# Kernel tuning notes

Measured on AMD Instinct MI355X. Metric: run time of the kernel, lower is better.

## Reference

```python
import jax, jax.numpy as jnp
import numpy as np

B, TQ, TK, D, V = 16, 64, 512, 256, 32000


def setup_inputs() -> dict:
    key = jax.random.key(0)
    k = jax.random.split(key, 8)
    return {
        "domainslots": jax.random.normal(k[0], (B, TQ, D), jnp.float32),
        "out_states": jax.random.normal(k[1], (B, TQ, D), jnp.float32),
        "context": jax.random.normal(k[2], (B, TK, D), jnp.float32),
        "context_plain": jax.random.randint(k[3], (B, TK), 0, V, jnp.int64 if jax.config.jax_enable_x64 else jnp.int32),
        "W_state": jax.random.normal(k[4], (D, V), jnp.float32) * 0.02,
        "b_state": jnp.zeros((V,), jnp.float32),
        "W_gen": jax.random.normal(k[5], (3 * D, 1), jnp.float32) * 0.02,
        "b_gen": jnp.zeros((1,), jnp.float32),
    }


def reference(domainslots, out_states, context, context_plain, W_state, b_state, W_gen, b_gen):
    d = out_states.shape[-1]
    # pointer attention: softmax(Q K^T / sqrt(d)) over context  -> [B, TQ, TK]
    scores = jnp.einsum("bqd,bkd->bqk", out_states, context) / jnp.sqrt(jnp.asarray(d, out_states.dtype))
    pointer_attn = jax.nn.softmax(scores, axis=-1)

    # generation distribution over vocab  -> [B, TQ, V]
    p_state_vocab = jax.nn.softmax(out_states @ W_state + b_state, axis=-1)

    # copy distribution: scatter-add attention mass onto source token ids
    b_idx = jnp.arange(B)[:, None, None]           # [B,1,1]
    q_idx = jnp.arange(TQ)[None, :, None]          # [1,TQ,1]
    v_idx = context_plain[:, None, :]              # [B,1,TK] broadcast over TQ
    p_state_ptr = jnp.zeros((B, TQ, V), p_state_vocab.dtype).at[b_idx, q_idx, v_idx].add(pointer_attn)

    # attention-weighted context vector  -> [B, TQ, D]
    context_vec = jnp.einsum("bqk,bkd->bqd", pointer_attn, context)

    # generation gate  -> [B, TQ, 1]
    p_gen_vec = jnp.concatenate([out_states, context_vec, domainslots], axis=-1)
    p_state_gen = jax.nn.sigmoid(p_gen_vec @ W_gen + b_gen)

    p_state_out = p_state_gen * p_state_vocab + (1.0 - p_state_gen) * p_state_ptr
    return jnp.log(p_state_out)
```

## Files before the change

### kernel.cpp

```cpp
#include <hip/hip_runtime.h>
#include <math.h>

typedef short short8 __attribute__((ext_vector_type(8)));
typedef float f32x4 __attribute__((ext_vector_type(4)));

#define B_ 16
#define TQ_ 64
#define TK_ 512
#define D_ 256
#define V_ 32000
#define M_ (B_ * TQ_)

__device__ __forceinline__ unsigned short f2bf(float x) {
    unsigned int u = __float_as_uint(x);
    unsigned int r = (u + 0x7fffu + ((u >> 16) & 1u)) >> 16;
    return (unsigned short)r;
}

__device__ __forceinline__ void gload_lds16(const void* g, void* l) {
    __builtin_amdgcn_global_load_lds(
        (const __attribute__((address_space(1))) void*)g,
        (__attribute__((address_space(3))) void*)l, 16, 0, 0);
}

__global__ __launch_bounds__(256) void dedup_kernel(
    const int* __restrict__ cp, int* __restrict__ nexta, int* __restrict__ leader)
{
    __shared__ __align__(16) int c[TK_];
    const int b = blockIdx.x, tid = threadIdx.x;
    c[tid] = cp[b * TK_ + tid];
    c[tid + 256] = cp[b * TK_ + 256 + tid];
    __syncthreads();
    for (int k = tid; k < TK_; k += 256) {
        const int v = c[k];
        int fm = 1024, nx = 1024;
#pragma unroll 8
        for (int j0 = 0; j0 < TK_; j0 += 4) {
            const int4 q = *(const int4*)&c[j0];
            if (q.x == v) { fm = min(fm, j0);     if (j0     > k) nx = min(nx, j0);     }
            if (q.y == v) { fm = min(fm, j0 + 1); if (j0 + 1 > k) nx = min(nx, j0 + 1); }
            if (q.z == v) { fm = min(fm, j0 + 2); if (j0 + 2 > k) nx = min(nx, j0 + 2); }
            if (q.w == v) { fm = min(fm, j0 + 3); if (j0 + 3 > k) nx = min(nx, j0 + 3); }
        }
        nexta[b * TK_ + k] = (nx < 1024) ? nx : -1;
        leader[b * TK_ + k] = (fm == k) ? 1 : 0;
    }
}

__global__ __launch_bounds__(256) void conv_a_kernel(
    const float* __restrict__ A, unsigned short* __restrict__ Ab)
{
    const int i = (blockIdx.x * 256 + threadIdx.x) * 4;
    const float4 v = *(const float4*)&A[i];
    ushort4 o;
    o.x = f2bf(v.x); o.y = f2bf(v.y); o.z = f2bf(v.z); o.w = f2bf(v.w);
    *(ushort4*)&Ab[i] = o;
}

__global__ __launch_bounds__(256) void conv_w_kernel(
    const float* __restrict__ W, unsigned short* __restrict__ Wt)
{
    __shared__ float tile[64][65];
    const int tid = threadIdx.x;
    const int k0 = (blockIdx.x & 3) * 64;
    const int n0 = (blockIdx.x >> 2) * 64;
#pragma unroll
    for (int i = 0; i < 16; i++) {
        const int r = i * 4 + (tid >> 6), cc = tid & 63;
        tile[r][cc] = W[(k0 + r) * V_ + n0 + cc];
    }
    __syncthreads();
#pragma unroll
    for (int i = 0; i < 4; i++) {
        const int nl = i * 16 + (tid >> 4);
        const int kq = (tid & 15) * 4;
        ushort4 o;
        o.x = f2bf(tile[kq + 0][nl]);
        o.y = f2bf(tile[kq + 1][nl]);
        o.z = f2bf(tile[kq + 2][nl]);
        o.w = f2bf(tile[kq + 3][nl]);
        *(ushort4*)&Wt[(n0 + nl) * D_ + k0 + kq] = o;
    }
}

__global__ __launch_bounds__(256) void conv_c_kernel(
    const float* __restrict__ ctx, unsigned short* __restrict__ Cb,
    unsigned short* __restrict__ Ct)
{
    __shared__ float tile[64][65];
    const int tid = threadIdx.x;
    const int b = blockIdx.x >> 5;
    const int r5 = blockIdx.x & 31;
    const int k0 = (r5 >> 2) * 64;
    const int d0 = (r5 & 3) * 64;
#pragma unroll
    for (int i = 0; i < 16; i++) {
        const int r = i * 4 + (tid >> 6), cc = tid & 63;
        const float v = ctx[((b * TK_) + k0 + r) * D_ + d0 + cc];
        tile[r][cc] = v;
        Cb[((b * TK_) + k0 + r) * D_ + d0 + cc] = f2bf(v);
    }
    __syncthreads();
#pragma unroll
    for (int i = 0; i < 4; i++) {
        const int dl = i * 16 + (tid >> 4);
        const int kq = (tid & 15) * 4;
        ushort4 o;
        o.x = f2bf(tile[kq + 0][dl]);
        o.y = f2bf(tile[kq + 1][dl]);
        o.z = f2bf(tile[kq + 2][dl]);
        o.w = f2bf(tile[kq + 3][dl]);
        *(ushort4*)&Ct[((b * D_) + d0 + dl) * TK_ + k0 + kq] = o;
    }
}

template <int LDA, int LDB, int KTOT>
__global__ __launch_bounds__(256) void gemm_small(
    const unsigned short* __restrict__ A,
    const unsigned short* __restrict__ Bt,
    float* __restrict__ C, int ldc, int nchunks, int btrows, float scale)
{
    __shared__ short Al[64][72];
    __shared__ short Bl[128][72];
    const int tid = threadIdx.x;
    const int b = blockIdx.x / nchunks;
    const int n0 = (blockIdx.x % nchunks) * 128;
    A += (size_t)b * 64 * LDA;
    Bt += (size_t)b * btrows * LDB;
    C += (size_t)b * 64 * ldc;

    const int wid = tid >> 6;
    const int lane = tid & 63;
    const int wm = wid & 1, wn = wid >> 1;
    const int quad = lane >> 4, l15 = lane & 15;

    f32x4 acc[2][4];
#pragma unroll
    for (int i = 0; i < 2; i++)
#pragma unroll
        for (int j = 0; j < 4; j++) acc[i][j] = f32x4{0.f, 0.f, 0.f, 0.f};

    for (int k0 = 0; k0 < KTOT; k0 += 64) {
        __syncthreads();
#pragma unroll
        for (int i = 0; i < 2; i++) {
            const int c = tid + i * 256;
            const int r = c >> 3, kc = (c & 7) * 8;
            *(uint4*)&Al[r][kc] = *(const uint4*)&A[r * LDA + k0 + kc];
        }
#pragma unroll
        for (int i = 0; i < 4; i++) {
            const int c = tid + i * 256;
            const int r = c >> 3, kc = (c & 7) * 8;
            *(uint4*)&Bl[r][kc] = *(const uint4*)&Bt[(n0 + r) * LDB + k0 + kc];
        }
        __syncthreads();
#pragma unroll
        for (int ks = 0; ks < 64; ks += 32) {
            short8 af[2], bf[4];
#pragma unroll
            for (int mt = 0; mt < 2; mt++)
                af[mt] = *(const short8*)&Al[wm * 32 + mt * 16 + l15][ks + quad * 8];
#pragma unroll
            for (int nt = 0; nt < 4; nt++)
                bf[nt] = *(const short8*)&Bl[wn * 64 + nt * 16 + l15][ks + quad * 8];
#pragma unroll
            for (int mt = 0; mt < 2; mt++)
#pragma unroll
                for (int nt = 0; nt < 4; nt++)
                    acc[mt][nt] = __builtin_amdgcn_mfma_f32_16x16x32_bf16(
                        af[mt], bf[nt], acc[mt][nt], 0, 0, 0);
        }
    }
#pragma unroll
    for (int mt = 0; mt < 2; mt++)
#pragma unroll
        for (int nt = 0; nt < 4; nt++)
#pragma unroll
            for (int r = 0; r < 4; r++) {
                const int rl = wm * 32 + mt * 16 + quad * 4 + r;
                const int col = n0 + wn * 64 + nt * 16 + l15;
                C[rl * ldc + col] = acc[mt][nt][r] * scale;
            }
}

__global__ __launch_bounds__(256) void softmax_kernel(
    float* __restrict__ S, unsigned short* __restrict__ Pb)
{
    const int w = threadIdx.x >> 6, lane = threadIdx.x & 63;
    const int row = blockIdx.x * 4 + w;
    float v[8], m = -1e30f;
#pragma unroll
    for (int j = 0; j < 8; j++) { v[j] = S[row * TK_ + lane + 64 * j]; m = fmaxf(m, v[j]); }
#pragma unroll
    for (int off = 32; off; off >>= 1) m = fmaxf(m, __shfl_xor(m, off));
    float s = 0.f;
#pragma unroll
    for (int j = 0; j < 8; j++) { v[j] = __expf(v[j] - m); s += v[j]; }
#pragma unroll
    for (int off = 32; off; off >>= 1) s += __shfl_xor(s, off);
    const float inv = 1.0f / s;
#pragma unroll
    for (int j = 0; j < 8; j++) {
        const float p = v[j] * inv;
        S[row * TK_ + lane + 64 * j] = p;
        Pb[row * TK_ + lane + 64 * j] = f2bf(p);
    }
}

__global__ __launch_bounds__(256) void pgen_kernel(
    const float* __restrict__ os, const float* __restrict__ cv,
    const float* __restrict__ dm, const float* __restrict__ W_gen,
    const float* __restrict__ b_gen, float* __restrict__ pg)
{
    const int w = threadIdx.x >> 6, lane = threadIdx.x & 63;
    const int row = blockIdx.x * 4 + w;
    const int d4 = lane * 4;
    const float4 o4 = *(const float4*)&os[row * D_ + d4];
    const float4 c4 = *(const float4*)&cv[row * D_ + d4];
    const float4 m4 = *(const float4*)&dm[row * D_ + d4];
    const float4 w0 = *(const float4*)&W_gen[d4];
    const float4 w1 = *(const float4*)&W_gen[D_ + d4];
    const float4 w2 = *(const float4*)&W_gen[2 * D_ + d4];
    float p = o4.x * w0.x + o4.y * w0.y + o4.z * w0.z + o4.w * w0.w
            + c4.x * w1.x + c4.y * w1.y + c4.z * w1.z + c4.w * w1.w
            + m4.x * w2.x + m4.y * w2.y + m4.z * w2.z + m4.w * w2.w;
#pragma unroll
    for (int off = 32; off; off >>= 1) p += __shfl_xor(p, off);
    if (lane == 0) pg[row] = 1.0f / (1.0f + __expf(-(p + b_gen[0])));
}

__global__ __launch_bounds__(256) void gemm_vocab_z(
    const unsigned short* __restrict__ A,
    const unsigned short* __restrict__ Bt,
    const float* __restrict__ b_state,
    float* __restrict__ Z)
{
    __shared__ short Al[128][64];
    __shared__ short Bl[128][64];
    __shared__ float bst[128];

    const int tid = threadIdx.x;
    const int swz = (blockIdx.x & 7) * 250 + (blockIdx.x >> 3);
    const int m0 = (swz & 7) * 128;
    const int n0 = (swz >> 3) * 128;

    if (tid < 128) bst[tid] = b_state[n0 + tid];

    const int wid = tid >> 6, lane = tid & 63;
    const int wm = wid & 1, wn = wid >> 1;
    const int quad = lane >> 4, l15 = lane & 15;
    const int srow = lane >> 3;
    const int scolz = ((lane & 7) ^ srow) << 3;

    f32x4 acc[4][4];
#pragma unroll
    for (int i = 0; i < 4; i++)
#pragma unroll
        for (int j = 0; j < 4; j++) acc[i][j] = f32x4{0.f, 0.f, 0.f, 0.f};

    for (int k0 = 0; k0 < D_; k0 += 64) {
        __syncthreads();
#pragma unroll
        for (int j = 0; j < 4; j++) {
            const int c = j * 4 + wid;
            const int r = c * 8 + srow;
            gload_lds16(&A[(size_t)(m0 + r) * D_ + k0 + scolz], &Al[c * 8][0]);
        }
#pragma unroll
        for (int j = 0; j < 4; j++) {
            const int c = j * 4 + wid;
            const int r = c * 8 + srow;
            gload_lds16(&Bt[(size_t)(n0 + r) * D_ + k0 + scolz], &Bl[c * 8][0]);
        }
        __syncthreads();
#pragma unroll
        for (int ks = 0; ks < 64; ks += 32) {
            short8 af[4], bf[4];
#pragma unroll
            for (int mt = 0; mt < 4; mt++) {
                const int row = wm * 64 + mt * 16 + l15;
                af[mt] = *(const short8*)&Al[row][(ks + quad * 8) ^ ((l15 & 7) << 3)];
            }
#pragma unroll
            for (int nt = 0; nt < 4; nt++) {
                const int row = wn * 64 + nt * 16 + l15;
                bf[nt] = *(const short8*)&Bl[row][(ks + quad * 8) ^ ((l15 & 7) << 3)];
            }
#pragma unroll
            for (int mt = 0; mt < 4; mt++)
#pragma unroll
                for (int nt = 0; nt < 4; nt++)
                    acc[mt][nt] = __builtin_amdgcn_mfma_f32_16x16x32_bf16(
                        af[mt], bf[nt], acc[mt][nt], 0, 0, 0);
        }
    }

#pragma unroll
    for (int mt = 0; mt < 4; mt++) {
        float rs[4] = {0.f, 0.f, 0.f, 0.f};
#pragma unroll
        for (int nt = 0; nt < 4; nt++) {
            const float bcol = bst[wn * 64 + nt * 16 + l15];
#pragma unroll
            for (int r = 0; r < 4; r++)
                rs[r] += __expf(acc[mt][nt][r] + bcol);
        }
#pragma unroll
        for (int r = 0; r < 4; r++) {
            float v = rs[r];
            v += __shfl_xor(v, 1);
            v += __shfl_xor(v, 2);
            v += __shfl_xor(v, 4);
            v += __shfl_xor(v, 8);
            if (l15 == 0)
                atomicAdd(&Z[m0 + wm * 64 + mt * 16 + quad * 4 + r], v);
        }
    }
}

__global__ __launch_bounds__(256) void gemm_vocab_out(
    const unsigned short* __restrict__ A,
    const unsigned short* __restrict__ Bt,
    const float* __restrict__ b_state,
    const float* __restrict__ pg,
    const float* __restrict__ Z,
    float* __restrict__ out)
{
    __shared__ short Al[128][64];
    __shared__ short Bl[128][64];
    __shared__ float bst[128];
    __shared__ float rcs[128];

    const int tid = threadIdx.x;
    const int swz = (blockIdx.x & 7) * 250 + (blockIdx.x >> 3);
    const int m0 = (swz & 7) * 128;
    const int n0 = (swz >> 3) * 128;

    if (tid < 128) {
        bst[tid] = b_state[n0 + tid];
        rcs[tid] = logf(pg[m0 + tid]) - logf(Z[m0 + tid]);
    }

    const int wid = tid >> 6, lane = tid & 63;
    const int wm = wid & 1, wn = wid >> 1;
    const int quad = lane >> 4, l15 = lane & 15;
    const int srow = lane >> 3;
    const int scolz = ((lane & 7) ^ srow) << 3;

    f32x4 acc[4][4];
#pragma unroll
    for (int i = 0; i < 4; i++)
#pragma unroll
        for (int j = 0; j < 4; j++) acc[i][j] = f32x4{0.f, 0.f, 0.f, 0.f};

    for (int k0 = 0; k0 < D_; k0 += 64) {
        __syncthreads();
#pragma unroll
        for (int j = 0; j < 4; j++) {
            const int c = j * 4 + wid;
            const int r = c * 8 + srow;
            gload_lds16(&A[(size_t)(m0 + r) * D_ + k0 + scolz], &Al[c * 8][0]);
        }
#pragma unroll
        for (int j = 0; j < 4; j++) {
            const int c = j * 4 + wid;
            const int r = c * 8 + srow;
            gload_lds16(&Bt[(size_t)(n0 + r) * D_ + k0 + scolz], &Bl[c * 8][0]);
        }
        __syncthreads();
#pragma unroll
        for (int ks = 0; ks < 64; ks += 32) {
            short8 af[4], bf[4];
#pragma unroll
            for (int mt = 0; mt < 4; mt++) {
                const int row = wm * 64 + mt * 16 + l15;
                af[mt] = *(const short8*)&Al[row][(ks + quad * 8) ^ ((l15 & 7) << 3)];
            }
#pragma unroll
            for (int nt = 0; nt < 4; nt++) {
                const int row = wn * 64 + nt * 16 + l15;
                bf[nt] = *(const short8*)&Bl[row][(ks + quad * 8) ^ ((l15 & 7) << 3)];
            }
#pragma unroll
            for (int mt = 0; mt < 4; mt++)
#pragma unroll
                for (int nt = 0; nt < 4; nt++)
                    acc[mt][nt] = __builtin_amdgcn_mfma_f32_16x16x32_bf16(
                        af[mt], bf[nt], acc[mt][nt], 0, 0, 0);
        }
    }

#pragma unroll
    for (int mt = 0; mt < 4; mt++) {
#pragma unroll
        for (int nt = 0; nt < 4; nt++) {
            const float bcol = bst[wn * 64 + nt * 16 + l15];
#pragma unroll
            for (int r = 0; r < 4; r++) {
                const int row = wm * 64 + mt * 16 + quad * 4 + r;
                const int col = wn * 64 + nt * 16 + l15;
                out[(size_t)(m0 + row) * V_ + n0 + col] = acc[mt][nt][r] + bcol + rcs[row];
            }
        }
    }
}

__global__ __launch_bounds__(256) void fixup_kernel(
    const int* __restrict__ cp, const int* __restrict__ nexta,
    const int* __restrict__ leader, const float* __restrict__ attn,
    const float* __restrict__ pg, float* __restrict__ out)
{
    const int t = blockIdx.x * 256 + threadIdx.x;
    const int row = t >> 9, k = t & 511;
    const int b = row >> 6;
    if (!leader[b * TK_ + k]) return;
    float a = attn[row * TK_ + k];
    int j = nexta[b * TK_ + k];
    while (j >= 0) { a += attn[row * TK_ + j]; j = nexta[b * TK_ + j]; }
    const float val = (1.0f - pg[row]) * a;
    const int v = cp[b * TK_ + k];
    const size_t idx = (size_t)row * V_ + v;
    out[idx] = logf(expf(out[idx]) + val);
}

extern "C" void kernel_launch(void* const* d_in, const int* in_sizes, int n_in,
                              void* d_out, int out_size, void* d_ws, size_t ws_size,
                              hipStream_t stream)
{
    const float* domainslots = (const float*)d_in[0];
    const float* out_states  = (const float*)d_in[1];
    const float* context     = (const float*)d_in[2];
    const int*   cp          = (const int*)d_in[3];
    const float* W_state     = (const float*)d_in[4];
    const float* b_state     = (const float*)d_in[5];
    const float* W_gen       = (const float*)d_in[6];
    const float* b_gen       = (const float*)d_in[7];
    float* out = (float*)d_out;
    char* ws = (char*)d_ws;

    float* Z      = (float*)(ws);
    float* pg     = (float*)(ws + 4096);
    float* S      = (float*)(ws + 12288);
    int* nexta    = (int*)(ws + 2109440);
    int* leader   = (int*)(ws + 2142208);
    unsigned short* Ab = (unsigned short*)(ws + 2174976);
    unsigned short* Wt = (unsigned short*)(ws + 2699264);
    unsigned short* Cb = (unsigned short*)(ws + 19083264);
    unsigned short* Ct = (unsigned short*)(ws + 23277568);
    unsigned short* Pb = (unsigned short*)(ws + 27471872);
    float* cv     = (float*)(ws + 28520448);

    hipMemsetAsync(Z, 0, M_ * sizeof(float), stream);
    dedup_kernel<<<B_, 256, 0, stream>>>(cp, nexta, leader);
    conv_a_kernel<<<(M_ * D_) / 1024, 256, 0, stream>>>(out_states, Ab);
    conv_w_kernel<<<(D_ / 64) * (V_ / 64), 256, 0, stream>>>(W_state, Wt);
    conv_c_kernel<<<B_ * 32, 256, 0, stream>>>(context, Cb, Ct);

    gemm_small<D_, D_, D_><<<B_ * 4, 256, 0, stream>>>(Ab, Cb, S, TK_, 4, TK_, 0.0625f);
    softmax_kernel<<<M_ / 4, 256, 0, stream>>>(S, Pb);
    gemm_small<TK_, TK_, TK_><<<B_ * 2, 256, 0, stream>>>(Pb, Ct, cv, D_, 2, D_, 1.0f);
    pgen_kernel<<<M_ / 4, 256, 0, stream>>>(out_states, cv, domainslots, W_gen, b_gen, pg);

    gemm_vocab_z<<<(M_ / 128) * (V_ / 128), 256, 0, stream>>>(Ab, Wt, b_state, Z);
    gemm_vocab_out<<<(M_ / 128) * (V_ / 128), 256, 0, stream>>>(Ab, Wt, b_state, pg, Z, out);
    fixup_kernel<<<(M_ * TK_) / 256, 256, 0, stream>>>(cp, nexta, leader, S, pg, out);
}
```

Before: 325.9 us.

## Merge prep kernels, fuse softmax with PV gemm and gate dot, nontemporal output stores

Four conversion and dedup kernels are merged into one launch with block-range dispatch. Softmax, the attention-times-context MFMA gemm and the context part of the generation-gate dot product are fused into one kernel that keeps bf16 probabilities in LDS and accumulates gate partials with atomics, so the cv and Pb intermediates are never written. The large output store in the vocab gemm now uses nontemporal stores to avoid cache pollution. The fused kernel recomputes softmax four times per batch (once per d-slice) and runs only 64 blocks, which can limit parallelism.

```diff
diff --git a/kernel.cpp b/kernel.cpp
--- a/kernel.cpp
+++ b/kernel.cpp
@@ -23,94 +23,88 @@
         (__attribute__((address_space(3))) void*)l, 16, 0, 0);
 }
 
-__global__ __launch_bounds__(256) void dedup_kernel(
+__global__ __launch_bounds__(256) void prep_kernel(
+    const float* __restrict__ W, unsigned short* __restrict__ Wt,
+    const float* __restrict__ ctx, unsigned short* __restrict__ Cb,
+    unsigned short* __restrict__ Ct,
+    const float* __restrict__ A, unsigned short* __restrict__ Ab,
     const int* __restrict__ cp, int* __restrict__ nexta, int* __restrict__ leader)
 {
+    __shared__ float tile[64][65];
     __shared__ __align__(16) int c[TK_];
-    const int b = blockIdx.x, tid = threadIdx.x;
-    c[tid] = cp[b * TK_ + tid];
-    c[tid + 256] = cp[b * TK_ + 256 + tid];
-    __syncthreads();
-    for (int k = tid; k < TK_; k += 256) {
-        const int v = c[k];
-        int fm = 1024, nx = 1024;
+    const int bid = blockIdx.x;
+    const int tid = threadIdx.x;
+
+    if (bid < 2000) {
+        const int k0 = (bid & 3) * 64;
+        const int n0 = (bid >> 2) * 64;
+#pragma unroll
+        for (int i = 0; i < 16; i++) {
+            const int r = i * 4 + (tid >> 6), cc = tid & 63;
+            tile[r][cc] = W[(k0 + r) * V_ + n0 + cc];
+        }
+        __syncthreads();
+#pragma unroll
+        for (int i = 0; i < 4; i++) {
+            const int nl = i * 16 + (tid >> 4);
+            const int kq = (tid & 15) * 4;
+            ushort4 o;
+            o.x = f2bf(tile[kq + 0][nl]);
+            o.y = f2bf(tile[kq + 1][nl]);
+            o.z = f2bf(tile[kq + 2][nl]);
+            o.w = f2bf(tile[kq + 3][nl]);
+            *(ushort4*)&Wt[(n0 + nl) * D_ + k0 + kq] = o;
+        }
+    } else if (bid < 2512) {
+        const int cbid = bid - 2000;
+        const int b = cbid >> 5;
+        const int r5 = cbid & 31;
+        const int k0 = (r5 >> 2) * 64;
+        const int d0 = (r5 & 3) * 64;
+#pragma unroll
+        for (int i = 0; i < 16; i++) {
+            const int r = i * 4 + (tid >> 6), cc = tid & 63;
+            const float v = ctx[((b * TK_) + k0 + r) * D_ + d0 + cc];
+            tile[r][cc] = v;
+            Cb[((b * TK_) + k0 + r) * D_ + d0 + cc] = f2bf(v);
+        }
+        __syncthreads();
+#pragma unroll
+        for (int i = 0; i < 4; i++) {
+            const int dl = i * 16 + (tid >> 4);
+            const int kq = (tid & 15) * 4;
+            ushort4 o;
+            o.x = f2bf(tile[kq + 0][dl]);
+            o.y = f2bf(tile[kq + 1][dl]);
+            o.z = f2bf(tile[kq + 2][dl]);
+            o.w = f2bf(tile[kq + 3][dl]);
+            *(ushort4*)&Ct[((b * D_) + d0 + dl) * TK_ + k0 + kq] = o;
+        }
+    } else if (bid < 2768) {
+        const int i = ((bid - 2512) * 256 + tid) * 4;
+        const float4 v = *(const float4*)&A[i];
+        ushort4 o;
+        o.x = f2bf(v.x); o.y = f2bf(v.y); o.z = f2bf(v.z); o.w = f2bf(v.w);
+        *(ushort4*)&Ab[i] = o;
+    } else {
+        const int b = bid - 2768;
+        c[tid] = cp[b * TK_ + tid];
+        c[tid + 256] = cp[b * TK_ + 256 + tid];
+        __syncthreads();
+        for (int k = tid; k < TK_; k += 256) {
+            const int v = c[k];
+            int fm = 1024, nx = 1024;
 #pragma unroll 8
-        for (int j0 = 0; j0 < TK_; j0 += 4) {
-            const int4 q = *(const int4*)&c[j0];
-            if (q.x == v) { fm = min(fm, j0);     if (j0     > k) nx = min(nx, j0);     }
-            if (q.y == v) { fm = min(fm, j0 + 1); if (j0 + 1 > k) nx = min(nx, j0 + 1); }
-            if (q.z == v) { fm = min(fm, j0 + 2); if (j0 + 2 > k) nx = min(nx, j0 + 2); }
-            if (q.w == v) { fm = min(fm, j0 + 3); if (j0 + 3 > k) nx = min(nx, j0 + 3); }
-        }
-        nexta[b * TK_ + k] = (nx < 1024) ? nx : -1;
-        leader[b * TK_ + k] = (fm == k) ? 1 : 0;
-    }
-}
-
-__global__ __launch_bounds__(256) void conv_a_kernel(
-    const float* __restrict__ A, unsigned short* __restrict__ Ab)
-{
-    const int i = (blockIdx.x * 256 + threadIdx.x) * 4;
-    const float4 v = *(const float4*)&A[i];
-    ushort4 o;
-    o.x = f2bf(v.x); o.y = f2bf(v.y); o.z = f2bf(v.z); o.w = f2bf(v.w);
-    *(ushort4*)&Ab[i] = o;
-}
-
-__global__ __launch_bounds__(256) void conv_w_kernel(
-    const float* __restrict__ W, unsigned short* __restrict__ Wt)
-{
-    __shared__ float tile[64][65];
-    const int tid = threadIdx.x;
-    const int k0 = (blockIdx.x & 3) * 64;
-    const int n0 = (blockIdx.x >> 2) * 64;
-#pragma unroll
-    for (int i = 0; i < 16; i++) {
-        const int r = i * 4 + (tid >> 6), cc = tid & 63;
-        tile[r][cc] = W[(k0 + r) * V_ + n0 + cc];
-    }
-    __syncthreads();
-#pragma unroll
-    for (int i = 0; i < 4; i++) {
-        const int nl = i * 16 + (tid >> 4);
-        const int kq = (tid & 15) * 4;
-        ushort4 o;
-        o.x = f2bf(tile[kq + 0][nl]);
-        o.y = f2bf(tile[kq + 1][nl]);
-        o.z = f2bf(tile[kq + 2][nl]);
-        o.w = f2bf(tile[kq + 3][nl]);
-        *(ushort4*)&Wt[(n0 + nl) * D_ + k0 + kq] = o;
-    }
-}
-
-__global__ __launch_bounds__(256) void conv_c_kernel(
-    const float* __restrict__ ctx, unsigned short* __restrict__ Cb,
-    unsigned short* __restrict__ Ct)
-{
-    __shared__ float tile[64][65];
-    const int tid = threadIdx.x;
-    const int b = blockIdx.x >> 5;
-    const int r5 = blockIdx.x & 31;
-    const int k0 = (r5 >> 2) * 64;
-    const int d0 = (r5 & 3) * 64;
-#pragma unroll
-    for (int i = 0; i < 16; i++) {
-        const int r = i * 4 + (tid >> 6), cc = tid & 63;
-        const float v = ctx[((b * TK_) + k0 + r) * D_ + d0 + cc];
-        tile[r][cc] = v;
-        Cb[((b * TK_) + k0 + r) * D_ + d0 + cc] = f2bf(v);
-    }
-    __syncthreads();
-#pragma unroll
-    for (int i = 0; i < 4; i++) {
-        const int dl = i * 16 + (tid >> 4);
-        const int kq = (tid & 15) * 4;
-        ushort4 o;
-        o.x = f2bf(tile[kq + 0][dl]);
-        o.y = f2bf(tile[kq + 1][dl]);
-        o.z = f2bf(tile[kq + 2][dl]);
-        o.w = f2bf(tile[kq + 3][dl]);
-        *(ushort4*)&Ct[((b * D_) + d0 + dl) * TK_ + k0 + kq] = o;
+            for (int j0 = 0; j0 < TK_; j0 += 4) {
+                const int4 q = *(const int4*)&c[j0];
+                if (q.x == v) { fm = min(fm, j0);     if (j0     > k) nx = min(nx, j0);     }
+                if (q.y == v) { fm = min(fm, j0 + 1); if (j0 + 1 > k) nx = min(nx, j0 + 1); }
+                if (q.z == v) { fm = min(fm, j0 + 2); if (j0 + 2 > k) nx = min(nx, j0 + 2); }
+                if (q.w == v) { fm = min(fm, j0 + 3); if (j0 + 3 > k) nx = min(nx, j0 + 3); }
+            }
+            nexta[b * TK_ + k] = (nx < 1024) ? nx : -1;
+            leader[b * TK_ + k] = (fm == k) ? 1 : 0;
+        }
     }
 }
 
@@ -184,50 +178,103 @@
             }
 }
 
-__global__ __launch_bounds__(256) void softmax_kernel(
-    float* __restrict__ S, unsigned short* __restrict__ Pb)
-{
-    const int w = threadIdx.x >> 6, lane = threadIdx.x & 63;
-    const int row = blockIdx.x * 4 + w;
-    float v[8], m = -1e30f;
-#pragma unroll
-    for (int j = 0; j < 8; j++) { v[j] = S[row * TK_ + lane + 64 * j]; m = fmaxf(m, v[j]); }
-#pragma unroll
-    for (int off = 32; off; off >>= 1) m = fmaxf(m, __shfl_xor(m, off));
-    float s = 0.f;
-#pragma unroll
-    for (int j = 0; j < 8; j++) { v[j] = __expf(v[j] - m); s += v[j]; }
-#pragma unroll
-    for (int off = 32; off; off >>= 1) s += __shfl_xor(s, off);
-    const float inv = 1.0f / s;
-#pragma unroll
-    for (int j = 0; j < 8; j++) {
-        const float p = v[j] * inv;
-        S[row * TK_ + lane + 64 * j] = p;
-        Pb[row * TK_ + lane + 64 * j] = f2bf(p);
-    }
-}
-
-__global__ __launch_bounds__(256) void pgen_kernel(
-    const float* __restrict__ os, const float* __restrict__ cv,
-    const float* __restrict__ dm, const float* __restrict__ W_gen,
-    const float* __restrict__ b_gen, float* __restrict__ pg)
+__global__ __launch_bounds__(256) void pv_fused(
+    const float* __restrict__ S,
+    float* __restrict__ attnP,
+    const unsigned short* __restrict__ Ct,
+    const float* __restrict__ W_gen,
+    float* __restrict__ pgacc)
+{
+    __shared__ __align__(16) unsigned short P[64][520];
+    const int tid = threadIdx.x;
+    const int b = blockIdx.x >> 2;
+    const int d0 = (blockIdx.x & 3) * 64;
+    const int w = tid >> 6, lane = tid & 63;
+
+    for (int qi = 0; qi < 16; ++qi) {
+        const int q = w * 16 + qi;
+        const int row = b * 64 + q;
+        float v[8], m = -1e30f;
+#pragma unroll
+        for (int j = 0; j < 8; j++) { v[j] = S[row * TK_ + lane + 64 * j]; m = fmaxf(m, v[j]); }
+#pragma unroll
+        for (int off = 32; off; off >>= 1) m = fmaxf(m, __shfl_xor(m, off));
+        float s = 0.f;
+#pragma unroll
+        for (int j = 0; j < 8; j++) { v[j] = __expf(v[j] - m); s += v[j]; }
+#pragma unroll
+        for (int off = 32; off; off >>= 1) s += __shfl_xor(s, off);
+        const float inv = 1.0f / s;
+#pragma unroll
+        for (int j = 0; j < 8; j++) {
+            const float p = v[j] * inv;
+            P[q][lane + 64 * j] = f2bf(p);
+            if (d0 == 0) attnP[row * TK_ + lane + 64 * j] = p;
+        }
+    }
+    __syncthreads();
+
+    const int wm = w & 1, wn = w >> 1;
+    const int quad = lane >> 4, l15 = lane & 15;
+    f32x4 acc[2][2];
+#pragma unroll
+    for (int i = 0; i < 2; i++)
+#pragma unroll
+        for (int j = 0; j < 2; j++) acc[i][j] = f32x4{0.f, 0.f, 0.f, 0.f};
+
+    const unsigned short* Cg = Ct + ((size_t)b * D_ + d0) * TK_;
+#pragma unroll
+    for (int k0 = 0; k0 < TK_; k0 += 32) {
+        short8 af[2], bf[2];
+#pragma unroll
+        for (int mt = 0; mt < 2; mt++)
+            af[mt] = *(const short8*)&P[wm * 32 + mt * 16 + l15][k0 + quad * 8];
+#pragma unroll
+        for (int nt = 0; nt < 2; nt++)
+            bf[nt] = *(const short8*)&Cg[(size_t)(wn * 32 + nt * 16 + l15) * TK_ + k0 + quad * 8];
+#pragma unroll
+        for (int mt = 0; mt < 2; mt++)
+#pragma unroll
+            for (int nt = 0; nt < 2; nt++)
+                acc[mt][nt] = __builtin_amdgcn_mfma_f32_16x16x32_bf16(
+                    af[mt], bf[nt], acc[mt][nt], 0, 0, 0);
+    }
+
+    float wg1v[2];
+#pragma unroll
+    for (int nt = 0; nt < 2; nt++)
+        wg1v[nt] = W_gen[D_ + d0 + wn * 32 + nt * 16 + l15];
+#pragma unroll
+    for (int mt = 0; mt < 2; mt++)
+#pragma unroll
+        for (int r = 0; r < 4; r++) {
+            const int row = wm * 32 + mt * 16 + quad * 4 + r;
+            float val = acc[mt][0][r] * wg1v[0] + acc[mt][1][r] * wg1v[1];
+            val += __shfl_xor(val, 1);
+            val += __shfl_xor(val, 2);
+            val += __shfl_xor(val, 4);
+            val += __shfl_xor(val, 8);
+            if (l15 == 0) atomicAdd(&pgacc[b * 64 + row], val);
+        }
+}
+
+__global__ __launch_bounds__(256) void pgen_fin(
+    const float* __restrict__ os, const float* __restrict__ dm,
+    const float* __restrict__ W_gen, const float* __restrict__ b_gen,
+    const float* __restrict__ pgacc, float* __restrict__ pg)
 {
     const int w = threadIdx.x >> 6, lane = threadIdx.x & 63;
     const int row = blockIdx.x * 4 + w;
     const int d4 = lane * 4;
     const float4 o4 = *(const float4*)&os[row * D_ + d4];
-    const float4 c4 = *(const float4*)&cv[row * D_ + d4];
     const float4 m4 = *(const float4*)&dm[row * D_ + d4];
     const float4 w0 = *(const float4*)&W_gen[d4];
-    const float4 w1 = *(const float4*)&W_gen[D_ + d4];
     const float4 w2 = *(const float4*)&W_gen[2 * D_ + d4];
     float p = o4.x * w0.x + o4.y * w0.y + o4.z * w0.z + o4.w * w0.w
-            + c4.x * w1.x + c4.y * w1.y + c4.z * w1.z + c4.w * w1.w
             + m4.x * w2.x + m4.y * w2.y + m4.z * w2.z + m4.w * w2.w;
 #pragma unroll
     for (int off = 32; off; off >>= 1) p += __shfl_xor(p, off);
-    if (lane == 0) pg[row] = 1.0f / (1.0f + __expf(-(p + b_gen[0])));
+    if (lane == 0) pg[row] = 1.0f / (1.0f + __expf(-(p + pgacc[row] + b_gen[0])));
 }
 
 __global__ __launch_bounds__(256) void gemm_vocab_z(
@@ -400,7 +447,9 @@
             for (int r = 0; r < 4; r++) {
                 const int row = wm * 64 + mt * 16 + quad * 4 + r;
                 const int col = wn * 64 + nt * 16 + l15;
-                out[(size_t)(m0 + row) * V_ + n0 + col] = acc[mt][nt][r] + bcol + rcs[row];
+                __builtin_nontemporal_store(
+                    acc[mt][nt][r] + bcol + rcs[row],
+                    &out[(size_t)(m0 + row) * V_ + n0 + col]);
             }
         }
     }
@@ -440,7 +489,8 @@
     char* ws = (char*)d_ws;
 
     float* Z      = (float*)(ws);
-    float* pg     = (float*)(ws + 4096);
+    float* pgacc  = (float*)(ws + 4096);
+    float* pg     = (float*)(ws + 8192);
     float* S      = (float*)(ws + 12288);
     int* nexta    = (int*)(ws + 2109440);
     int* leader   = (int*)(ws + 2142208);
@@ -448,21 +498,19 @@
     unsigned short* Wt = (unsigned short*)(ws + 2699264);
     unsigned short* Cb = (unsigned short*)(ws + 19083264);
     unsigned short* Ct = (unsigned short*)(ws + 23277568);
-    unsigned short* Pb = (unsigned short*)(ws + 27471872);
-    float* cv     = (float*)(ws + 28520448);
-
-    hipMemsetAsync(Z, 0, M_ * sizeof(float), stream);
-    dedup_kernel<<<B_, 256, 0, stream>>>(cp, nexta, leader);
-    conv_a_kernel<<<(M_ * D_) / 1024, 256, 0, stream>>>(out_states, Ab);
-    conv_w_kernel<<<(D_ / 64) * (V_ / 64), 256, 0, stream>>>(W_state, Wt);
-    conv_c_kernel<<<B_ * 32, 256, 0, stream>>>(context, Cb, Ct);
+    float* attnP  = (float*)(ws + 27471872);
+
+    hipMemsetAsync(ws, 0, 8192, stream);
+
+    prep_kernel<<<2784, 256, 0, stream>>>(W_state, Wt, context, Cb, Ct,
+                                          out_states, Ab, cp, nexta, leader);
 
     gemm_small<D_, D_, D_><<<B_ * 4, 256, 0, stream>>>(Ab, Cb, S, TK_, 4, TK_, 0.0625f);
-    softmax_kernel<<<M_ / 4, 256, 0, stream>>>(S, Pb);
-    gemm_small<TK_, TK_, TK_><<<B_ * 2, 256, 0, stream>>>(Pb, Ct, cv, D_, 2, D_, 1.0f);
-    pgen_kernel<<<M_ / 4, 256, 0, stream>>>(out_states, cv, domainslots, W_gen, b_gen, pg);
+
+    pv_fused<<<B_ * 4, 256, 0, stream>>>(S, attnP, Ct, W_gen, pgacc);
+    pgen_fin<<<M_ / 4, 256, 0, stream>>>(out_states, domainslots, W_gen, b_gen, pgacc, pg);
 
     gemm_vocab_z<<<(M_ / 128) * (V_ / 128), 256, 0, stream>>>(Ab, Wt, b_state, Z);
     gemm_vocab_out<<<(M_ / 128) * (V_ / 128), 256, 0, stream>>>(Ab, Wt, b_state, pg, Z, out);
-    fixup_kernel<<<(M_ * TK_) / 256, 256, 0, stream>>>(cp, nexta, leader, S, pg, out);
-}
+    fixup_kernel<<<(M_ * TK_) / 256, 256, 0, stream>>>(cp, nexta, leader, attnP, pg, out);
+}
```

Result: slower. 365.1 us (+12.0%).
